# Kernel tuning notes

Hardware: AMD Instinct MI355X
Metric: run time of the kernel (lower is better)

## Reference

```python
import jax, jax.numpy as jnp
import numpy as np

N_NODES = 100000
N_EDGES = 1600000
F_IN, HID, N_CLS = 128, 64, 40


def gcn_conv(x, src, dst, W, b, n_nodes):
    # x: [N, Fin] -> [N, Fout]; edges already include self-loops.
    h = x @ W  # [N, Fout]
    ones = jnp.ones_like(src, dtype=h.dtype)
    deg = jax.ops.segment_sum(ones, dst, num_segments=n_nodes)  # [N]
    dinv = jnp.where(deg > 0, jax.lax.rsqrt(deg), 0.0)
    norm = dinv[src] * dinv[dst]  # [E]
    msg = h[src] * norm[:, None]  # gather + scale
    out = jax.ops.segment_sum(msg, dst, num_segments=n_nodes)  # scatter-sum
    return out + b


def setup_inputs() -> dict:
    key = jax.random.key(0)
    ks = jax.random.split(key, 8)
    x = jax.random.normal(ks[0], (N_NODES, F_IN), dtype=jnp.float32)
    edge_index = jax.random.randint(ks[1], (2, N_EDGES), 0, N_NODES, dtype=jnp.int64)

    def glorot(k, fi, fo):
        s = float(np.sqrt(6.0 / (fi + fo)))
        return jax.random.uniform(k, (fi, fo), jnp.float32, -s, s)

    return {
        "x": x,
        "edge_index": edge_index,
        "W1": glorot(ks[2], F_IN, HID), "b1": jnp.zeros((HID,), jnp.float32),
        "W2": glorot(ks[3], HID, HID), "b2": jnp.zeros((HID,), jnp.float32),
        "W3": glorot(ks[4], HID, N_CLS), "b3": jnp.zeros((N_CLS,), jnp.float32),
    }


def reference(x, edge_index, W1, b1, W2, b2, W3, b3):
    n = x.shape[0]
    loop = jnp.arange(n, dtype=edge_index.dtype)
    src = jnp.concatenate([edge_index[0], loop])  # add self-loops
    dst = jnp.concatenate([edge_index[1], loop])
    # layer 1..3: GCNConv -> relu -> dropout(eval: identity)
    h = jax.nn.relu(gcn_conv(x, src, dst, W1, b1, n))
    h = jax.nn.relu(gcn_conv(h, src, dst, W2, b2, n))
    h = jax.nn.relu(gcn_conv(h, src, dst, W3, b3, n))
    return jax.nn.log_softmax(h, axis=1)
```

## Files before the change

### kernel.cpp

```cpp
#include <hip/hip_runtime.h>
#include <math.h>

typedef _Float16 half8   __attribute__((ext_vector_type(8)));
typedef float    float4v __attribute__((ext_vector_type(4)));

#define CAP 6144

static __device__ __forceinline__ unsigned short f32_to_f16u(float f) {
    _Float16 h = (_Float16)f;
    return __builtin_bit_cast(unsigned short, h);
}


__global__ __launch_bounds__(256) void prep_init(
    const float* __restrict__ W1, const float* __restrict__ W2, const float* __restrict__ W3,
    unsigned short* __restrict__ Wf1, unsigned short* __restrict__ Wf2,
    unsigned short* __restrict__ Wf3, int* __restrict__ bcur, int NB)
{
    if (blockIdx.x == 3) {
        for (int i = threadIdx.x; i < NB; i += 256) bcur[i] = 0;
        return;
    }
    const float* W; unsigned short* Wf; int K, M;
    if (blockIdx.x == 0)      { W = W1; Wf = Wf1; K = 128; M = 64; }
    else if (blockIdx.x == 1) { W = W2; Wf = Wf2; K = 64;  M = 64; }
    else                      { W = W3; Wf = Wf3; K = 64;  M = 40; }
    const int NT = (M + 15) >> 4, NTC = NT << 4, KS = K >> 5;
    for (int i = threadIdx.x; i < K * NTC; i += 256) {
        int k = i / NTC, nn = i - k * NTC;
        unsigned short hv = 0;
        if (nn < M) hv = f32_to_f16u(W[(size_t)k * M + nn]);
        int s = k >> 5, q = (k >> 3) & 3, j = k & 7;
        int u = nn >> 4, lane = (q << 4) | (nn & 15);
        Wf[((u * KS + s) << 9) + (lane << 3) + j] = hv;
    }
}


__global__ __launch_bounds__(256) void bin_edges(
    const int* __restrict__ src, const int* __restrict__ dst,
    int* __restrict__ bcur, unsigned int* __restrict__ bint, int E, int NB)
{
    __shared__ int h[512];
    __shared__ int rbase[512];
    const int tid = threadIdx.x;
    h[tid] = 0; h[tid + 256] = 0;
    __syncthreads();
    const int eb = blockIdx.x * 4096 + tid;
    int d[16], sr[16];
    #pragma unroll
    for (int k = 0; k < 16; ++k) {
        int i = eb + k * 256;
        if (i < E) {
            d[k] = dst[i]; sr[k] = src[i];
            atomicAdd(&h[d[k] >> 8], 1);
        } else d[k] = -1;
    }
    __syncthreads();
    for (int j = tid; j < NB; j += 256) {
        int c = h[j];
        rbase[j] = c ? atomicAdd(&bcur[j], c) : 0;
        h[j] = 0;
    }
    __syncthreads();
    #pragma unroll
    for (int k = 0; k < 16; ++k) {
        if (d[k] >= 0) {
            int bkt = d[k] >> 8;
            int pos = rbase[bkt] + atomicAdd(&h[bkt], 1);
            if (pos < CAP)
                bint[(size_t)bkt * CAP + pos] =
                    ((unsigned int)sr[k] << 8) | (unsigned int)(d[k] & 255);
        }
    }
}


__global__ __launch_bounds__(256) void build_csr(
    const unsigned int* __restrict__ bint, const int* __restrict__ bcur,
    int2* __restrict__ rp2, float* __restrict__ dinv, int* __restrict__ es, int n)
{
    __shared__ int cnt[256];
    __shared__ int sc[256];
    __shared__ int cur[256];
    const int b = blockIdx.x, tid = threadIdx.x;
    int total = bcur[b]; if (total > CAP) total = CAP;
    const unsigned int* bp = bint + (size_t)b * CAP;
    int* ep = es + (size_t)b * CAP;
    const int base = b * CAP;

    cnt[tid] = 0;
    __syncthreads();
    for (int i = tid; i < total; i += 256)
        atomicAdd(&cnt[bp[i] & 255], 1);
    __syncthreads();

    int v = cnt[tid];
    sc[tid] = v;
    __syncthreads();
    for (int off = 1; off < 256; off <<= 1) {
        int x = (tid >= off) ? sc[tid - off] : 0;
        __syncthreads();
        sc[tid] += x;
        __syncthreads();
    }
    int excl = sc[tid] - v;
    int node = (b << 8) + tid;
    if (node < n) {
        rp2[node]  = make_int2(base + excl, base + excl + v);
        dinv[node] = rsqrtf((float)(v + 1));
    }
    cur[tid] = excl;
    __syncthreads();

    for (int i = tid; i < total; i += 256) {
        unsigned int p = bp[i];
        int pos = atomicAdd(&cur[p & 255], 1);
        ep[pos] = (int)(p >> 8);
    }
}


template<int KK, int NT, int STRIDE, int MOUT>
__global__ __launch_bounds__(256) void gemm_t(
    const float* __restrict__ Xin, const unsigned short* __restrict__ Wf,
    const float* __restrict__ dinv, unsigned short* __restrict__ H, int n)
{
    constexpr int KS = KK >> 5;
    __shared__ __align__(16) unsigned short ldsA[4 * KS * 512];
    const int tid = threadIdx.x;
    const int n0  = blockIdx.x * 64;

    half8 bf[NT * KS];
    {
        const int lane = tid & 63;
        #pragma unroll
        for (int u = 0; u < NT; ++u)
            #pragma unroll
            for (int s = 0; s < KS; ++s)
                bf[u * KS + s] = *(const half8*)&Wf[((u * KS + s) << 9) + (lane << 3)];
    }

    {
        const int rl = tid >> 3;
        const int kl = tid & 7;
        #pragma unroll
        for (int rb = 0; rb < 64; rb += 32) {
            int r = rl + rb;
            int node = n0 + r;
            int t = r >> 4, m = r & 15;
            #pragma unroll
            for (int kq8 = 0; kq8 < (KK >> 2); kq8 += 8) {
                int k0 = (kl + kq8) << 2;
                unsigned short h[4] = {0, 0, 0, 0};
                if (node < n) {
                    const float* xp = Xin + (size_t)node * KK + k0;
                    float4v v = *(const float4v*)xp;
                    #pragma unroll
                    for (int i = 0; i < 4; ++i) h[i] = f32_to_f16u(v[i]);
                }
                int s = k0 >> 5, q = (k0 >> 3) & 3, j0 = k0 & 7;
                int lane = (q << 4) | m;
                unsigned short* p = &ldsA[((t * KS + s) << 9) + (lane << 3) + j0];
                unsigned int lo = (unsigned int)h[0] | ((unsigned int)h[1] << 16);
                unsigned int hi = (unsigned int)h[2] | ((unsigned int)h[3] << 16);
                *(uint2*)p = make_uint2(lo, hi);
            }
        }
    }

    __syncthreads();

    const int wv   = tid >> 6;
    const int lane = tid & 63;
    float4v acc[NT];
    #pragma unroll
    for (int u = 0; u < NT; ++u) acc[u] = (float4v){0.f, 0.f, 0.f, 0.f};

    #pragma unroll
    for (int s = 0; s < KS; ++s) {
        half8 a = *(const half8*)&ldsA[((wv * KS + s) << 9) + (lane << 3)];
        #pragma unroll
        for (int u = 0; u < NT; ++u)
            acc[u] = __builtin_amdgcn_mfma_f32_16x16x32_f16(a, bf[u * KS + s], acc[u], 0, 0, 0);
    }

    const int mcol = lane & 15;
    const int quad = lane >> 4;
    #pragma unroll
    for (int reg = 0; reg < 4; ++reg) {
        int node = n0 + (wv << 4) + (quad << 2) + reg;
        if (node >= n) continue;
        float dv = dinv[node];
        #pragma unroll
        for (int u = 0; u < NT; ++u) {
            int col = (u << 4) + mcol;
            if (col < MOUT)
                H[(size_t)node * STRIDE + col] = f32_to_f16u(acc[u][reg] * dv);
        }
    }
}


template<int NT, int STRIDE, int MOUT>
__global__ __launch_bounds__(256) void gather_gemm(
    const int2* __restrict__ rp2, const int* __restrict__ es,
    const unsigned short* __restrict__ Hin, const float* __restrict__ dinv,
    const float* __restrict__ bias, const unsigned short* __restrict__ Wf,
    unsigned short* __restrict__ Hout, int n)
{
    constexpr int KS = 2;
    __shared__ __align__(16) unsigned short ldsA[4 * KS * 512];
    const int tid  = threadIdx.x;
    const int wv   = tid >> 6;
    const int lane = tid & 63;
    const int nw0  = blockIdx.x * 64 + (wv << 4);

    half8 bf[NT * KS];
    #pragma unroll
    for (int u = 0; u < NT; ++u)
        #pragma unroll
        for (int s = 0; s < KS; ++s)
            bf[u * KS + s] = *(const half8*)&Wf[((u * KS + s) << 9) + (lane << 3)];

    const int half   = lane >> 5;
    const int lane32 = lane & 31;
    const int slot   = (lane >> 3) & 3;
    const int c8     = lane & 7;
    const uint4* H4  = (const uint4*)Hin;

    float bi[8];
    #pragma unroll
    for (int i = 0; i < 8; ++i) bi[i] = bias[(c8 << 3) + i];

    const half8 hz = {(_Float16)0, (_Float16)0, (_Float16)0, (_Float16)0,
                      (_Float16)0, (_Float16)0, (_Float16)0, (_Float16)0};

    for (int p = 0; p < 8; ++p) {
        const int node = nw0 + (p << 1) + half;
        half8 hacc = hz;
        float dv = 0.0f;
        if (node < n) {
            dv = dinv[node];
            const int2 e = rp2[node];
            if (slot == 0) hacc = __builtin_bit_cast(half8, H4[(size_t)node * 8 + c8]);
            for (int cb = e.x; cb < e.y; cb += 32) {
                const int rem = e.y - cb;
                int eidx = cb + lane32; if (eidx > e.y - 1) eidx = e.y - 1;
                const int ei = es[eidx];
                #pragma unroll
                for (int j = 0; j < 8; ++j) {
                    const int idx = (j << 2) + slot;
                    const int s = __shfl(ei, (half << 5) + idx, 64);
                    if (idx < rem)
                        hacc = hacc + __builtin_bit_cast(half8, H4[(size_t)s * 8 + c8]);
                }
            }
        }
        #pragma unroll
        for (int step = 8; step <= 16; step <<= 1) {
            uint4 u = __builtin_bit_cast(uint4, hacc);
            uint4 o;
            o.x = __shfl_xor(u.x, step, 64);
            o.y = __shfl_xor(u.y, step, 64);
            o.z = __shfl_xor(u.z, step, 64);
            o.w = __shfl_xor(u.w, step, 64);
            hacc = hacc + __builtin_bit_cast(half8, o);
        }
        if (slot == 0) {
            unsigned short o[8];
            #pragma unroll
            for (int i = 0; i < 8; ++i)
                o[i] = f32_to_f16u(fmaxf((float)hacc[i] * dv + bi[i], 0.0f));
            uint4 w;
            w.x = (unsigned int)o[0] | ((unsigned int)o[1] << 16);
            w.y = (unsigned int)o[2] | ((unsigned int)o[3] << 16);
            w.z = (unsigned int)o[4] | ((unsigned int)o[5] << 16);
            w.w = (unsigned int)o[6] | ((unsigned int)o[7] << 16);
            const int m = (p << 1) | half;
            unsigned short* dst =
                &ldsA[((wv * KS + (c8 >> 2)) << 9) + ((((c8 & 3) << 4) | m) << 3)];
            *(uint4*)dst = w;
        }
    }

    float4v acc[NT];
    #pragma unroll
    for (int u = 0; u < NT; ++u) acc[u] = (float4v){0.f, 0.f, 0.f, 0.f};

    #pragma unroll
    for (int s = 0; s < KS; ++s) {
        half8 a = *(const half8*)&ldsA[((wv * KS + s) << 9) + (lane << 3)];
        #pragma unroll
        for (int u = 0; u < NT; ++u)
            acc[u] = __builtin_amdgcn_mfma_f32_16x16x32_f16(a, bf[u * KS + s], acc[u], 0, 0, 0);
    }

    const int mcol = lane & 15;
    const int quad = lane >> 4;
    #pragma unroll
    for (int reg = 0; reg < 4; ++reg) {
        int node = nw0 + (quad << 2) + reg;
        if (node >= n) continue;
        float dv = dinv[node];
        #pragma unroll
        for (int u = 0; u < NT; ++u) {
            int col = (u << 4) + mcol;
            if (col < MOUT)
                Hout[(size_t)node * STRIDE + col] = f32_to_f16u(acc[u][reg] * dv);
        }
    }
}


template<int MOUT, int ROWU4>
__global__ __launch_bounds__(256) void gather_softmax(
    const int2* __restrict__ rp2, const int* __restrict__ es,
    const unsigned short* __restrict__ H, const float* __restrict__ dinv,
    const float* __restrict__ bias, float* __restrict__ out, int n)
{
    const int lane   = threadIdx.x & 63;
    const int half   = lane >> 5;
    const int lane32 = lane & 31;
    const int slot   = (lane >> 3) & 3;
    const int c8     = lane & 7;
    const bool act   = c8 < ROWU4;
    const uint4* H4  = (const uint4*)H;

    float bi[8];
    #pragma unroll
    for (int i = 0; i < 8; ++i) {
        int col = (c8 << 3) + i;
        bi[i] = (col < MOUT) ? bias[col] : 0.0f;
    }

    const half8 hz = {(_Float16)0, (_Float16)0, (_Float16)0, (_Float16)0,
                      (_Float16)0, (_Float16)0, (_Float16)0, (_Float16)0};

    const int TW2 = (int)(gridDim.x << 3);
    for (int nb = (((int)blockIdx.x << 2) + ((int)threadIdx.x >> 6)) << 1; nb < n; nb += TW2) {
        const int node = nb + half;
        const int2 e = rp2[node];
        const float dv = dinv[node];

        half8 hacc = hz;
        if (slot == 0 && act)
            hacc = __builtin_bit_cast(half8, H4[(size_t)node * ROWU4 + c8]);

        for (int cb = e.x; cb < e.y; cb += 32) {
            const int rem = e.y - cb;
            int eidx = cb + lane32; if (eidx > e.y - 1) eidx = e.y - 1;
            const int ei = es[eidx];
            #pragma unroll
            for (int j = 0; j < 8; ++j) {
                const int idx = (j << 2) + slot;
                const int s = __shfl(ei, (half << 5) + idx, 64);
                if (idx < rem && act)
                    hacc = hacc + __builtin_bit_cast(half8, H4[(size_t)s * ROWU4 + c8]);
            }
        }

        #pragma unroll
        for (int step = 8; step <= 16; step <<= 1) {
            uint4 u = __builtin_bit_cast(uint4, hacc);
            uint4 o;
            o.x = __shfl_xor(u.x, step, 64);
            o.y = __shfl_xor(u.y, step, 64);
            o.z = __shfl_xor(u.z, step, 64);
            o.w = __shfl_xor(u.w, step, 64);
            hacc = hacc + __builtin_bit_cast(half8, o);
        }

        float z[8]; float m = -INFINITY;
        #pragma unroll
        for (int i = 0; i < 8; ++i) {
            int col = (c8 << 3) + i;
            z[i] = (col < MOUT && act) ? fmaxf((float)hacc[i] * dv + bi[i], 0.0f)
                                       : -INFINITY;
            m = fmaxf(m, z[i]);
        }
        m = fmaxf(m, __shfl_xor(m, 1, 64));
        m = fmaxf(m, __shfl_xor(m, 2, 64));
        m = fmaxf(m, __shfl_xor(m, 4, 64));
        float s = 0.0f;
        #pragma unroll
        for (int i = 0; i < 8; ++i) s += expf(z[i] - m);
        s += __shfl_xor(s, 1, 64);
        s += __shfl_xor(s, 2, 64);
        s += __shfl_xor(s, 4, 64);
        float ls = logf(s) + m;
        if (slot == 0 && c8 < (MOUT + 7) / 8) {
            float* op = out + (size_t)node * MOUT + (c8 << 3);
            float4v o0 = {z[0] - ls, z[1] - ls, z[2] - ls, z[3] - ls};
            float4v o1 = {z[4] - ls, z[5] - ls, z[6] - ls, z[7] - ls};
            *(float4v*)op = o0;
            *(float4v*)(op + 4) = o1;
        }
    }
}


extern "C" void kernel_launch(void* const* d_in, const int* in_sizes, int n_in,
                              void* d_out, int out_size, void* d_ws, size_t ws_size,
                              hipStream_t stream)
{
    const float* x  = (const float*)d_in[0];
    const int*   ei = (const int*)  d_in[1];
    const float* W1 = (const float*)d_in[2];
    const float* b1 = (const float*)d_in[3];
    const float* W2 = (const float*)d_in[4];
    const float* b2 = (const float*)d_in[5];
    const float* W3 = (const float*)d_in[6];
    const float* b3 = (const float*)d_in[7];

    const int F_IN = 128;
    const int n = in_sizes[0] / F_IN;
    const int E = in_sizes[1] / 2;
    const int* src = ei;
    const int* dst = ei + E;
    float* out = (float*)d_out;

    const int NB = (n + 255) >> 8;

    auto align = [](size_t v) { return (v + 255) & ~(size_t)255; };
    char* w = (char*)d_ws;
    size_t off = 0;
    float*          dinv = (float*)(w + off);          off = align(off + (size_t)n * 4);
    unsigned short* H1   = (unsigned short*)(w + off); off = align(off + (size_t)n * 64 * 2);
    unsigned short* H2   = (unsigned short*)(w + off); off = align(off + (size_t)n * 64 * 2);
    unsigned short* H3   = (unsigned short*)(w + off); off = align(off + (size_t)n * 40 * 2);
    int2*           rp2  = (int2*)(w + off);           off = align(off + (size_t)n * 8);
    int*            es   = (int*)(w + off);            off = align(off + (size_t)NB * CAP * 4);
    unsigned int*   bint = (unsigned int*)(w + off);   off = align(off + (size_t)NB * CAP * 4);
    int*            bcur = (int*)(w + off);            off = align(off + (size_t)512 * 4);
    unsigned short* Wf1  = (unsigned short*)(w + off); off = align(off + (size_t)8192 * 2);
    unsigned short* Wf2  = (unsigned short*)(w + off); off = align(off + (size_t)4096 * 2);
    unsigned short* Wf3  = (unsigned short*)(w + off); off = align(off + (size_t)3072 * 2);

    const int BLK = 256;
    auto cdiv = [](int a, int b) { return (a + b - 1) / b; };
    const int EB = cdiv(E, 4096);
    const int GB = cdiv(n, 64);
    const int GG = 2048;

    prep_init<<<4, BLK, 0, stream>>>(W1, W2, W3, Wf1, Wf2, Wf3, bcur, NB);
    bin_edges<<<EB, BLK, 0, stream>>>(src, dst, bcur, bint, E, NB);
    build_csr<<<NB, BLK, 0, stream>>>(bint, bcur, rp2, dinv, es, n);

    gemm_t<128, 4, 64, 64><<<GB, BLK, 0, stream>>>(x, Wf1, dinv, H1, n);

    gather_gemm<4, 64, 64><<<GB, BLK, 0, stream>>>(rp2, es, H1, dinv, b1, Wf2, H2, n);

    gather_gemm<3, 40, 40><<<GB, BLK, 0, stream>>>(rp2, es, H2, dinv, b2, Wf3, H3, n);

    gather_softmax<40, 5><<<GG, BLK, 0, stream>>>(rp2, es, H3, dinv, b3, out, n);
}
```

Baseline: 299.0 us.

## Split fused gather+GEMM kernels into grid-stride gather and separate fp16 GEMM

Replaces the fused gather_gemm kernels, which aggregated neighbours and then ran an MFMA transform per 64-node block, with a grid-stride gather kernel that writes the aggregated fp16 activations to global memory. A templated gemm_t that reads fp16 input then applies the next layer's weights. The aim is better load balancing on the irregular gather, using a fixed 2048-block grid-stride launch instead of one block per 64 nodes, and less register pressure from keeping MFMA weights live during the gather. In exchange it adds two kernel launches and an extra write and read of an N×64 fp16 intermediate. H2 aliases H1 to reuse the buffer.

```diff
diff --git a/kernel.cpp b/kernel.cpp
--- a/kernel.cpp
+++ b/kernel.cpp
@@ -121,9 +121,9 @@
 }
 
 
-template<int KK, int NT, int STRIDE, int MOUT>
+template<int KK, int NT, int STRIDE, int MOUT, bool INF32>
 __global__ __launch_bounds__(256) void gemm_t(
-    const float* __restrict__ Xin, const unsigned short* __restrict__ Wf,
+    const void* __restrict__ Xin, const unsigned short* __restrict__ Wf,
     const float* __restrict__ dinv, unsigned short* __restrict__ H, int n)
 {
     constexpr int KS = KK >> 5;
@@ -154,10 +154,20 @@
                 int k0 = (kl + kq8) << 2;
                 unsigned short h[4] = {0, 0, 0, 0};
                 if (node < n) {
-                    const float* xp = Xin + (size_t)node * KK + k0;
-                    float4v v = *(const float4v*)xp;
-                    #pragma unroll
-                    for (int i = 0; i < 4; ++i) h[i] = f32_to_f16u(v[i]);
+                    if (INF32) {
+                        const float* xp = (const float*)Xin + (size_t)node * KK + k0;
+                        float4v v = *(const float4v*)xp;
+                        #pragma unroll
+                        for (int i = 0; i < 4; ++i) h[i] = f32_to_f16u(v[i]);
+                    } else {
+                        const unsigned int* ap =
+                            (const unsigned int*)Xin + (((size_t)node * KK + k0) >> 1);
+                        uint2 v = *(const uint2*)ap;
+                        h[0] = (unsigned short)(v.x & 0xffff);
+                        h[1] = (unsigned short)(v.x >> 16);
+                        h[2] = (unsigned short)(v.y & 0xffff);
+                        h[3] = (unsigned short)(v.y >> 16);
+                    }
                 }
                 int s = k0 >> 5, q = (k0 >> 3) & 3, j0 = k0 & 7;
                 int lane = (q << 4) | m;
@@ -202,122 +212,11 @@
 }
 
 
-template<int NT, int STRIDE, int MOUT>
-__global__ __launch_bounds__(256) void gather_gemm(
-    const int2* __restrict__ rp2, const int* __restrict__ es,
-    const unsigned short* __restrict__ Hin, const float* __restrict__ dinv,
-    const float* __restrict__ bias, const unsigned short* __restrict__ Wf,
-    unsigned short* __restrict__ Hout, int n)
-{
-    constexpr int KS = 2;
-    __shared__ __align__(16) unsigned short ldsA[4 * KS * 512];
-    const int tid  = threadIdx.x;
-    const int wv   = tid >> 6;
-    const int lane = tid & 63;
-    const int nw0  = blockIdx.x * 64 + (wv << 4);
-
-    half8 bf[NT * KS];
-    #pragma unroll
-    for (int u = 0; u < NT; ++u)
-        #pragma unroll
-        for (int s = 0; s < KS; ++s)
-            bf[u * KS + s] = *(const half8*)&Wf[((u * KS + s) << 9) + (lane << 3)];
-
-    const int half   = lane >> 5;
-    const int lane32 = lane & 31;
-    const int slot   = (lane >> 3) & 3;
-    const int c8     = lane & 7;
-    const uint4* H4  = (const uint4*)Hin;
-
-    float bi[8];
-    #pragma unroll
-    for (int i = 0; i < 8; ++i) bi[i] = bias[(c8 << 3) + i];
-
-    const half8 hz = {(_Float16)0, (_Float16)0, (_Float16)0, (_Float16)0,
-                      (_Float16)0, (_Float16)0, (_Float16)0, (_Float16)0};
-
-    for (int p = 0; p < 8; ++p) {
-        const int node = nw0 + (p << 1) + half;
-        half8 hacc = hz;
-        float dv = 0.0f;
-        if (node < n) {
-            dv = dinv[node];
-            const int2 e = rp2[node];
-            if (slot == 0) hacc = __builtin_bit_cast(half8, H4[(size_t)node * 8 + c8]);
-            for (int cb = e.x; cb < e.y; cb += 32) {
-                const int rem = e.y - cb;
-                int eidx = cb + lane32; if (eidx > e.y - 1) eidx = e.y - 1;
-                const int ei = es[eidx];
-                #pragma unroll
-                for (int j = 0; j < 8; ++j) {
-                    const int idx = (j << 2) + slot;
-                    const int s = __shfl(ei, (half << 5) + idx, 64);
-                    if (idx < rem)
-                        hacc = hacc + __builtin_bit_cast(half8, H4[(size_t)s * 8 + c8]);
-                }
-            }
-        }
-        #pragma unroll
-        for (int step = 8; step <= 16; step <<= 1) {
-            uint4 u = __builtin_bit_cast(uint4, hacc);
-            uint4 o;
-            o.x = __shfl_xor(u.x, step, 64);
-            o.y = __shfl_xor(u.y, step, 64);
-            o.z = __shfl_xor(u.z, step, 64);
-            o.w = __shfl_xor(u.w, step, 64);
-            hacc = hacc + __builtin_bit_cast(half8, o);
-        }
-        if (slot == 0) {
-            unsigned short o[8];
-            #pragma unroll
-            for (int i = 0; i < 8; ++i)
-                o[i] = f32_to_f16u(fmaxf((float)hacc[i] * dv + bi[i], 0.0f));
-            uint4 w;
-            w.x = (unsigned int)o[0] | ((unsigned int)o[1] << 16);
-            w.y = (unsigned int)o[2] | ((unsigned int)o[3] << 16);
-            w.z = (unsigned int)o[4] | ((unsigned int)o[5] << 16);
-            w.w = (unsigned int)o[6] | ((unsigned int)o[7] << 16);
-            const int m = (p << 1) | half;
-            unsigned short* dst =
-                &ldsA[((wv * KS + (c8 >> 2)) << 9) + ((((c8 & 3) << 4) | m) << 3)];
-            *(uint4*)dst = w;
-        }
-    }
-
-    float4v acc[NT];
-    #pragma unroll
-    for (int u = 0; u < NT; ++u) acc[u] = (float4v){0.f, 0.f, 0.f, 0.f};
-
-    #pragma unroll
-    for (int s = 0; s < KS; ++s) {
-        half8 a = *(const half8*)&ldsA[((wv * KS + s) << 9) + (lane << 3)];
-        #pragma unroll
-        for (int u = 0; u < NT; ++u)
-            acc[u] = __builtin_amdgcn_mfma_f32_16x16x32_f16(a, bf[u * KS + s], acc[u], 0, 0, 0);
-    }
-
-    const int mcol = lane & 15;
-    const int quad = lane >> 4;
-    #pragma unroll
-    for (int reg = 0; reg < 4; ++reg) {
-        int node = nw0 + (quad << 2) + reg;
-        if (node >= n) continue;
-        float dv = dinv[node];
-        #pragma unroll
-        for (int u = 0; u < NT; ++u) {
-            int col = (u << 4) + mcol;
-            if (col < MOUT)
-                Hout[(size_t)node * STRIDE + col] = f32_to_f16u(acc[u][reg] * dv);
-        }
-    }
-}
-
-
 template<int MOUT, int ROWU4>
-__global__ __launch_bounds__(256) void gather_softmax(
+__global__ __launch_bounds__(256) void gather_t(
     const int2* __restrict__ rp2, const int* __restrict__ es,
     const unsigned short* __restrict__ H, const float* __restrict__ dinv,
-    const float* __restrict__ bias, float* __restrict__ out, int n)
+    const float* __restrict__ bias, unsigned short* __restrict__ Aout, int n)
 {
     const int lane   = threadIdx.x & 63;
     const int half   = lane >> 5;
@@ -329,10 +228,7 @@
 
     float bi[8];
     #pragma unroll
-    for (int i = 0; i < 8; ++i) {
-        int col = (c8 << 3) + i;
-        bi[i] = (col < MOUT) ? bias[col] : 0.0f;
-    }
+    for (int i = 0; i < 8; ++i) bi[i] = bias[(c8 << 3) + i];
 
     const half8 hz = {(_Float16)0, (_Float16)0, (_Float16)0, (_Float16)0,
                       (_Float16)0, (_Float16)0, (_Float16)0, (_Float16)0};
@@ -371,6 +267,80 @@
             hacc = hacc + __builtin_bit_cast(half8, o);
         }
 
+        if (slot == 0) {
+            unsigned short o[8];
+            #pragma unroll
+            for (int i = 0; i < 8; ++i)
+                o[i] = f32_to_f16u(fmaxf((float)hacc[i] * dv + bi[i], 0.0f));
+            uint4 w;
+            w.x = (unsigned int)o[0] | ((unsigned int)o[1] << 16);
+            w.y = (unsigned int)o[2] | ((unsigned int)o[3] << 16);
+            w.z = (unsigned int)o[4] | ((unsigned int)o[5] << 16);
+            w.w = (unsigned int)o[6] | ((unsigned int)o[7] << 16);
+            ((uint4*)Aout)[(size_t)node * 8 + c8] = w;
+        }
+    }
+}
+
+
+template<int MOUT, int ROWU4>
+__global__ __launch_bounds__(256) void gather_softmax(
+    const int2* __restrict__ rp2, const int* __restrict__ es,
+    const unsigned short* __restrict__ H, const float* __restrict__ dinv,
+    const float* __restrict__ bias, float* __restrict__ out, int n)
+{
+    const int lane   = threadIdx.x & 63;
+    const int half   = lane >> 5;
+    const int lane32 = lane & 31;
+    const int slot   = (lane >> 3) & 3;
+    const int c8     = lane & 7;
+    const bool act   = c8 < ROWU4;
+    const uint4* H4  = (const uint4*)H;
+
+    float bi[8];
+    #pragma unroll
+    for (int i = 0; i < 8; ++i) {
+        int col = (c8 << 3) + i;
+        bi[i] = (col < MOUT) ? bias[col] : 0.0f;
+    }
+
+    const half8 hz = {(_Float16)0, (_Float16)0, (_Float16)0, (_Float16)0,
+                      (_Float16)0, (_Float16)0, (_Float16)0, (_Float16)0};
+
+    const int TW2 = (int)(gridDim.x << 3);
+    for (int nb = (((int)blockIdx.x << 2) + ((int)threadIdx.x >> 6)) << 1; nb < n; nb += TW2) {
+        const int node = nb + half;
+        const int2 e = rp2[node];
+        const float dv = dinv[node];
+
+        half8 hacc = hz;
+        if (slot == 0 && act)
+            hacc = __builtin_bit_cast(half8, H4[(size_t)node * ROWU4 + c8]);
+
+        for (int cb = e.x; cb < e.y; cb += 32) {
+            const int rem = e.y - cb;
+            int eidx = cb + lane32; if (eidx > e.y - 1) eidx = e.y - 1;
+            const int ei = es[eidx];
+            #pragma unroll
+            for (int j = 0; j < 8; ++j) {
+                const int idx = (j << 2) + slot;
+                const int s = __shfl(ei, (half << 5) + idx, 64);
+                if (idx < rem && act)
+                    hacc = hacc + __builtin_bit_cast(half8, H4[(size_t)s * ROWU4 + c8]);
+            }
+        }
+
+        #pragma unroll
+        for (int step = 8; step <= 16; step <<= 1) {
+            uint4 u = __builtin_bit_cast(uint4, hacc);
+            uint4 o;
+            o.x = __shfl_xor(u.x, step, 64);
+            o.y = __shfl_xor(u.y, step, 64);
+            o.z = __shfl_xor(u.z, step, 64);
+            o.w = __shfl_xor(u.w, step, 64);
+            hacc = hacc + __builtin_bit_cast(half8, o);
+        }
+
         float z[8]; float m = -INFINITY;
         #pragma unroll
         for (int i = 0; i < 8; ++i) {
@@ -427,7 +397,7 @@
     size_t off = 0;
     float*          dinv = (float*)(w + off);          off = align(off + (size_t)n * 4);
     unsigned short* H1   = (unsigned short*)(w + off); off = align(off + (size_t)n * 64 * 2);
-    unsigned short* H2   = (unsigned short*)(w + off); off = align(off + (size_t)n * 64 * 2);
+    unsigned short* A    = (unsigned short*)(w + off); off = align(off + (size_t)n * 64 * 2);
     unsigned short* H3   = (unsigned short*)(w + off); off = align(off + (size_t)n * 40 * 2);
     int2*           rp2  = (int2*)(w + off);           off = align(off + (size_t)n * 8);
     int*            es   = (int*)(w + off);            off = align(off + (size_t)NB * CAP * 4);
@@ -436,6 +406,7 @@
     unsigned short* Wf1  = (unsigned short*)(w + off); off = align(off + (size_t)8192 * 2);
     unsigned short* Wf2  = (unsigned short*)(w + off); off = align(off + (size_t)4096 * 2);
     unsigned short* Wf3  = (unsigned short*)(w + off); off = align(off + (size_t)3072 * 2);
+    unsigned short* H2   = H1;
 
     const int BLK = 256;
     auto cdiv = [](int a, int b) { return (a + b - 1) / b; };
@@ -447,11 +418,12 @@
     bin_edges<<<EB, BLK, 0, stream>>>(src, dst, bcur, bint, E, NB);
     build_csr<<<NB, BLK, 0, stream>>>(bint, bcur, rp2, dinv, es, n);
 
-    gemm_t<128, 4, 64, 64><<<GB, BLK, 0, stream>>>(x, Wf1, dinv, H1, n);
-
-    gather_gemm<4, 64, 64><<<GB, BLK, 0, stream>>>(rp2, es, H1, dinv, b1, Wf2, H2, n);
-
-    gather_gemm<3, 40, 40><<<GB, BLK, 0, stream>>>(rp2, es, H2, dinv, b2, Wf3, H3, n);
-
+    gemm_t<128, 4, 64, 64, true><<<GB, BLK, 0, stream>>>(x, Wf1, dinv, H1, n);
+    gather_t<64, 8><<<GG, BLK, 0, stream>>>(rp2, es, H1, dinv, b1, A, n);
+
+    gemm_t<64, 4, 64, 64, false><<<GB, BLK, 0, stream>>>(A, Wf2, dinv, H2, n);
+    gather_t<64, 8><<<GG, BLK, 0, stream>>>(rp2, es, H2, dinv, b2, A, n);
+
+    gemm_t<64, 3, 40, 40, false><<<GB, BLK, 0, stream>>>(A, Wf3, dinv, H3, n);
     gather_softmax<40, 5><<<GG, BLK, 0, stream>>>(rp2, es, H3, dinv, b3, out, n);
 }
```

New measurement: 276.2 us (median of 2 runs). -7.6%, faster.
